# Optimization experiments

Measured on AMD Instinct MI355X. Metric: run time of the kernel, lower is better.

The kernel has to match this reference:

```python
import math
import jax, jax.numpy as jnp
import numpy as np

N_WL = 262144
T_REF = 273.15          # CONSTANTS.STANDARD_TEMPERATURE [K]
P_REF = 101325.0        # CONSTANTS.STANDARD_PRESSURE [Pa]
C_LIGHT = 2.99792458e8  # CONSTANTS.SPEED_OF_LIGHT
K_B = 1.380649e-23      # CONSTANTS.BOLTZMANN
N_AVO = 6.02214076e23   # CONSTANTS.AVOGADRO

# hard-coded line database: [center_wl, strength, width, temp_exp]; rows 0-2 O3, 3-5 H2O, 6-9 CO2
LINES = np.array([
    [254.0, 1.15e-17, 2.0, 0.05], [280.0, 5e-18, 3.0, 0.04], [310.0, 1.9e-19, 2.5, 0.03],
    [940.0, 2.5e-23, 3.0, 0.4],  [1130.0, 8.2e-24, 2.5, 0.35], [1380.0, 1.8e-22, 4.0, 0.45],
    [1400.0, 3.5e-25, 3.0, 0.5], [1600.0, 7.8e-26, 2.5, 0.48], [2000.0, 4.2e-24, 4.0, 0.52],
    [2700.0, 1.2e-24, 3.5, 0.49]], dtype=np.float32)
MASS = np.array([48.0]*3 + [18.0]*3 + [44.0]*4, dtype=np.float32)


def setup_inputs() -> dict:
    key = jax.random.key(0)
    ks = jax.random.split(key, 8)
    inp = {
        'wavelengths': jnp.linspace(200.0, 3000.0, N_WL, dtype=jnp.float32),
        'temperature': jnp.float32(250.0),
        'pressure': jnp.float32(80000.0),
        'conc_o3': jnp.float32(1e-6),
        'conc_h2o': jnp.float32(1e-2),
        'conc_co2': jnp.float32(4e-4),
        'mix_w1': jax.random.normal(ks[0], (10, 64), jnp.float32) * 0.3,
        'mix_b1': jnp.zeros((64,), jnp.float32),
        'mix_w2': jax.random.normal(ks[1], (64, 64), jnp.float32) * 0.12,
        'mix_b2': jnp.zeros((64,), jnp.float32),
        'mix_w3': jax.random.normal(ks[2], (64, N_WL), jnp.float32) * 0.12,
        'mix_b3': jnp.zeros((N_WL,), jnp.float32),
        'cont_w1': jax.random.normal(ks[3], (5, 32), jnp.float32) * 0.4,
        'cont_b1': jnp.zeros((32,), jnp.float32),
        'cont_w2': jax.random.normal(ks[4], (32, N_WL), jnp.float32) * 0.17,
        'cont_b2': jnp.zeros((N_WL,), jnp.float32),
    }
    return inp


def _voigt(wl, nu0, gamma_L, gamma_D):
    # wl: [N]; nu0, gamma_L, gamma_D: [L] -> returns [L, N]
    sigma = gamma_D / (math.sqrt(2.0 * math.log(2.0)) + 1e-12)          # [L]
    x = (wl[None, :] - nu0[:, None]) / (sigma[:, None] + 1e-12)          # [L,N]
    y = (gamma_L / (sigma + 1e-12))[:, None]                             # [L,1]
    t = y - 1j * x
    s = jnp.abs(x) + y
    mask1 = s >= 15.0
    mask2 = (s < 15.0) & (jnp.abs(x) >= 5.5)
    w1 = (t * 0.5641896 / (0.5 + t ** 2)).real
    u = t ** 2
    w2 = (t * (1.410474 + u * 0.5641896) / (0.75 + u * (3.0 + u))).real
    w3 = (jnp.exp(-x ** 2) * jnp.cos(2.0 * x * y) / math.sqrt(math.pi)
          + 2.0 * y / math.pi * jnp.sin(x ** 2) / (x ** 2 + y ** 2 + 1e-10))
    result = jnp.where(mask1, w1, jnp.where(mask2, w2, w3))
    return result / (sigma[:, None] * math.sqrt(math.pi) + 1e-12)


def reference(wavelengths, temperature, pressure, conc_o3, conc_h2o, conc_co2,
              mix_w1, mix_b1, mix_w2, mix_b2, mix_w3, mix_b3,
              cont_w1, cont_b1, cont_w2, cont_b2):
    lines = jnp.asarray(LINES)
    mass = jnp.asarray(MASS)
    conc = jnp.stack([conc_o3, conc_o3, conc_o3,
                      conc_h2o, conc_h2o, conc_h2o,
                      conc_co2, conc_co2, conc_co2, conc_co2])          # [10]
    nu0, strength, width, temp_exp = lines[:, 0], lines[:, 1], lines[:, 2], lines[:, 3]
    strength_T = strength * (T_REF / (temperature + 1e-12)) ** temp_exp  # [10]
    gamma_L = width * (pressure / (P_REF + 1e-12)) * jnp.sqrt(T_REF / (temperature + 1e-12))
    gamma_D = nu0 / C_LIGHT * jnp.sqrt(2.0 * K_B * temperature * N_AVO / (mass + 1e-12))

    profiles = _voigt(wavelengths, nu0, gamma_L, gamma_D)                # [10,N]
    cross = jnp.sum((conc * strength_T)[:, None] * profiles, axis=0)     # [N]

    # continuum net: 5 -> 32 (SiLU) -> N (softplus)
    cont_feat = jnp.stack([temperature / (T_REF + 1e-12),
                           pressure / (P_REF + 1e-12),
                           conc_h2o,
                           jnp.float32(1.0), jnp.float32(0.0)])
    h = jax.nn.silu(cont_feat @ cont_w1 + cont_b1)
    continuum = jax.nn.softplus(h @ cont_w2 + cont_b2)
    cross = cross + continuum

    # line-mixing net: 10 -> 64 (SiLU) -> 64 (SiLU) -> N (sigmoid); dropout is eval-mode identity
    mix_feat = jnp.concatenate([jnp.stack([temperature / (T_REF + 1e-12),
                                           pressure / (P_REF + 1e-12)]),
                                cross[:8]])
    m = jax.nn.silu(mix_feat @ mix_w1 + mix_b1)
    m = jax.nn.silu(m @ mix_w2 + mix_b2)
    mixing = jax.nn.sigmoid(m @ mix_w3 + mix_b3)
    return cross * (1.0 + 0.1 * (mixing - 0.5))
```

## Files before the change

### kernel.cpp

```cpp
#include <hip/hip_runtime.h>
#include <math.h>

#define N_WL 262144

#define T_REF 273.15
#define P_REF 101325.0
#define C_LIGHT 299792458.0
#define K_B 1.380649e-23
#define N_AVO 6.02214076e+23

__constant__ float c_nu0[10]  = {254.0f, 280.0f, 310.0f, 940.0f, 1130.0f, 1380.0f, 1400.0f, 1600.0f, 2000.0f, 2700.0f};
__constant__ float c_str[10]  = {1.15e-17f, 5e-18f, 1.9e-19f, 2.5e-23f, 8.2e-24f, 1.8e-22f, 3.5e-25f, 7.8e-26f, 4.2e-24f, 1.2e-24f};
__constant__ float c_wid[10]  = {2.0f, 3.0f, 2.5f, 3.0f, 2.5f, 4.0f, 3.0f, 2.5f, 4.0f, 3.5f};
__constant__ float c_texp[10] = {0.05f, 0.04f, 0.03f, 0.4f, 0.35f, 0.45f, 0.5f, 0.48f, 0.52f, 0.49f};
__constant__ float c_mass[10] = {48.f, 48.f, 48.f, 18.f, 18.f, 18.f, 44.f, 44.f, 44.f, 44.f};
__constant__ int   c_cidx[10] = {0, 0, 0, 1, 1, 1, 2, 2, 2, 2};

__device__ __forceinline__ float siluf(float x)     { return x / (1.0f + __expf(-x)); }
__device__ __forceinline__ float sigmoidf(float x)  { return 1.0f / (1.0f + __expf(-x)); }
__device__ __forceinline__ float softplusf(float x) { return fmaxf(x, 0.0f) + log1pf(expf(-fabsf(x))); }

__device__ __forceinline__ float voigt_w(float x, float y) {
    float ax = fabsf(x);
    float s  = ax + y;
    if (s >= 15.0f) {
        float ur = y * y - x * x;
        float ui = -2.0f * x * y;
        float dr = 0.5f + ur, di = ui;
        float nr = 0.5641896f * y, ni = 0.5641896f * (-x);
        float den = dr * dr + di * di;
        return (nr * dr + ni * di) / den;
    } else if (ax >= 5.5f) {
        float ur = y * y - x * x;
        float ui = -2.0f * x * y;
        float pr = 1.410474f + 0.5641896f * ur;
        float pi_ = 0.5641896f * ui;
        float tr = y, ti = -x;
        float nr = tr * pr - ti * pi_;
        float ni = tr * pi_ + ti * pr;
        float u2r = ur * ur - ui * ui;
        float u2i = 2.0f * ur * ui;
        float dr = 0.75f + 3.0f * ur + u2r;
        float di = 3.0f * ui + u2i;
        float den = dr * dr + di * di;
        return (nr * dr + ni * di) / den;
    } else {
        float x2 = x * x;
        return expf(-x2) * cosf(2.0f * x * y) * 0.5641895835477563f
             + (2.0f * y / 3.14159265358979f) * sinf(x2) / (x2 + y * y + 1e-10f);
    }
}

__global__ __launch_bounds__(256) void GasAbs_fused_kernel(
    const float* __restrict__ wl,
    const float* __restrict__ Tp, const float* __restrict__ Pp,
    const float* __restrict__ o3, const float* __restrict__ h2o, const float* __restrict__ co2,
    const float* __restrict__ mix_w1, const float* __restrict__ mix_b1,
    const float* __restrict__ mix_w2, const float* __restrict__ mix_b2,
    const float* __restrict__ mix_w3, const float* __restrict__ mix_b3,
    const float* __restrict__ cont_w1, const float* __restrict__ cont_b1,
    const float* __restrict__ cont_w2, const float* __restrict__ cont_b2,
    float* __restrict__ out)
{
    __shared__ float s_nu0[10], s_isig[10], s_y[10], s_scale[10];
    __shared__ float s_h[32];
    __shared__ float s_feat[10];
    __shared__ float s_m1[64];
    __shared__ float s_m2[64];

    const int t = threadIdx.x;

    if (t < 10) {
        const double T = (double)Tp[0];
        const double P = (double)Pp[0];
        const float cc3[3] = {o3[0], h2o[0], co2[0]};
        double nu0 = (double)c_nu0[t];
        double sT  = (double)c_str[t] * pow(T_REF / (T + 1e-12), (double)c_texp[t]);
        double gL  = (double)c_wid[t] * (P / (P_REF + 1e-12)) * sqrt(T_REF / (T + 1e-12));
        double gD  = nu0 / C_LIGHT * sqrt(2.0 * K_B * T * N_AVO / ((double)c_mass[t] + 1e-12));
        double sig = gD / (sqrt(2.0 * log(2.0)) + 1e-12);
        s_nu0[t]   = (float)nu0;
        s_isig[t]  = (float)(1.0 / (sig + 1e-12));
        s_y[t]     = (float)(gL / (sig + 1e-12));
        s_scale[t] = (float)((double)cc3[c_cidx[t]] * sT / (sig * sqrt(M_PI) + 1e-12));
    }
    if (t < 32) {
        const double T = (double)Tp[0];
        const double P = (double)Pp[0];
        float cf[5];
        cf[0] = (float)(T / (T_REF + 1e-12));
        cf[1] = (float)(P / (P_REF + 1e-12));
        cf[2] = h2o[0];
        cf[3] = 1.0f;
        cf[4] = 0.0f;
        float a = cont_b1[t];
        #pragma unroll
        for (int k = 0; k < 5; k++) a = fmaf(cf[k], cont_w1[k * 32 + t], a);
        s_h[t] = siluf(a);
    }
    __syncthreads();

    if (t < 8) {
        float w = wl[t];
        float c = cont_b2[t];
        #pragma unroll
        for (int j = 0; j < 32; j++) c = fmaf(s_h[j], cont_w2[(size_t)j * N_WL + t], c);
        float cross = softplusf(c);
        #pragma unroll
        for (int l = 0; l < 10; l++) {
            float x = (w - s_nu0[l]) * s_isig[l];
            cross = fmaf(s_scale[l], voigt_w(x, s_y[l]), cross);
        }
        s_feat[2 + t] = cross;
    }
    if (t == 0) {
        const double T = (double)Tp[0];
        const double P = (double)Pp[0];
        s_feat[0] = (float)(T / (T_REF + 1e-12));
        s_feat[1] = (float)(P / (P_REF + 1e-12));
    }
    __syncthreads();

    if (t < 64) {
        float a = mix_b1[t];
        #pragma unroll
        for (int k = 0; k < 10; k++) a = fmaf(s_feat[k], mix_w1[k * 64 + t], a);
        s_m1[t] = siluf(a);
    }
    __syncthreads();

    if (t < 64) {
        float a = mix_b2[t];
        #pragma unroll
        for (int k = 0; k < 64; k++) a = fmaf(s_m1[k], mix_w2[k * 64 + t], a);
        s_m2[t] = siluf(a);
    }
    __syncthreads();

    const int i0 = (blockIdx.x * 256 + t) * 4;

    const float4 w4 = *reinterpret_cast<const float4*>(wl + i0);

    float4 ac = *reinterpret_cast<const float4*>(cont_b2 + i0);
    #pragma unroll 16
    for (int j = 0; j < 32; j++) {
        const float hj = s_h[j];
        const float4 v = *reinterpret_cast<const float4*>(cont_w2 + (size_t)j * N_WL + i0);
        ac.x = fmaf(hj, v.x, ac.x);
        ac.y = fmaf(hj, v.y, ac.y);
        ac.z = fmaf(hj, v.z, ac.z);
        ac.w = fmaf(hj, v.w, ac.w);
    }

    float cr0 = softplusf(ac.x);
    float cr1 = softplusf(ac.y);
    float cr2 = softplusf(ac.z);
    float cr3 = softplusf(ac.w);

    #pragma unroll
    for (int l = 0; l < 10; l++) {
        const float nu0 = s_nu0[l], isig = s_isig[l], yy = s_y[l], sc = s_scale[l];
        cr0 = fmaf(sc, voigt_w((w4.x - nu0) * isig, yy), cr0);
        cr1 = fmaf(sc, voigt_w((w4.y - nu0) * isig, yy), cr1);
        cr2 = fmaf(sc, voigt_w((w4.z - nu0) * isig, yy), cr2);
        cr3 = fmaf(sc, voigt_w((w4.w - nu0) * isig, yy), cr3);
    }

    float4 am = *reinterpret_cast<const float4*>(mix_b3 + i0);
    #pragma unroll 16
    for (int j = 0; j < 64; j++) {
        const float mj = s_m2[j];
        const float4 v = *reinterpret_cast<const float4*>(mix_w3 + (size_t)j * N_WL + i0);
        am.x = fmaf(mj, v.x, am.x);
        am.y = fmaf(mj, v.y, am.y);
        am.z = fmaf(mj, v.z, am.z);
        am.w = fmaf(mj, v.w, am.w);
    }

    float4 o;
    o.x = cr0 * (0.95f + 0.1f * sigmoidf(am.x));
    o.y = cr1 * (0.95f + 0.1f * sigmoidf(am.y));
    o.z = cr2 * (0.95f + 0.1f * sigmoidf(am.z));
    o.w = cr3 * (0.95f + 0.1f * sigmoidf(am.w));
    *reinterpret_cast<float4*>(out + i0) = o;
}

extern "C" void kernel_launch(void* const* d_in, const int* in_sizes, int n_in,
                              void* d_out, int out_size, void* d_ws, size_t ws_size,
                              hipStream_t stream) {
    const float* wl      = (const float*)d_in[0];
    const float* Tp      = (const float*)d_in[1];
    const float* Pp      = (const float*)d_in[2];
    const float* o3      = (const float*)d_in[3];
    const float* h2o     = (const float*)d_in[4];
    const float* co2     = (const float*)d_in[5];
    const float* mix_w1  = (const float*)d_in[6];
    const float* mix_b1  = (const float*)d_in[7];
    const float* mix_w2  = (const float*)d_in[8];
    const float* mix_b2  = (const float*)d_in[9];
    const float* mix_w3  = (const float*)d_in[10];
    const float* mix_b3  = (const float*)d_in[11];
    const float* cont_w1 = (const float*)d_in[12];
    const float* cont_b1 = (const float*)d_in[13];
    const float* cont_w2 = (const float*)d_in[14];
    const float* cont_b2 = (const float*)d_in[15];
    float* out = (float*)d_out;

    const int threads = 256;
    const int blocks  = N_WL / (threads * 4);
    GasAbs_fused_kernel<<<blocks, threads, 0, stream>>>(
        wl, Tp, Pp, o3, h2o, co2,
        mix_w1, mix_b1, mix_w2, mix_b2, mix_w3, mix_b3,
        cont_w1, cont_b1, cont_w2, cont_b2, out);
}
```

Measured before the change: 153.8 us.

## Halve per-thread width and software-pipeline weight loads across Voigt compute

Each thread now handles 2 wavelengths instead of 4, doubling the block count from 256 to 512 so more of the GPU's compute units have work. Weight rows are loaded in batches of 8 float2s. The first batch of mix_w3 loads is issued before the Voigt computation so its memory latency overlaps that math, and each later batch is prefetched while the previous one is consumed. In exchange, every block repeats the small MLP prologue, which costs more in total, and the prefetch buffers raise register pressure.

```diff
diff --git a/kernel.cpp b/kernel.cpp
--- a/kernel.cpp
+++ b/kernel.cpp
@@ -137,52 +137,63 @@
     }
     __syncthreads();
 
-    const int i0 = (blockIdx.x * 256 + t) * 4;
-
-    const float4 w4 = *reinterpret_cast<const float4*>(wl + i0);
-
-    float4 ac = *reinterpret_cast<const float4*>(cont_b2 + i0);
-    #pragma unroll 16
-    for (int j = 0; j < 32; j++) {
-        const float hj = s_h[j];
-        const float4 v = *reinterpret_cast<const float4*>(cont_w2 + (size_t)j * N_WL + i0);
-        ac.x = fmaf(hj, v.x, ac.x);
-        ac.y = fmaf(hj, v.y, ac.y);
-        ac.z = fmaf(hj, v.z, ac.z);
-        ac.w = fmaf(hj, v.w, ac.w);
-    }
+    const int i0 = (blockIdx.x * 256 + t) * 2;
+
+    const float2 w2 = *reinterpret_cast<const float2*>(wl + i0);
+    float2 ac = *reinterpret_cast<const float2*>(cont_b2 + i0);
+    float2 am = *reinterpret_cast<const float2*>(mix_b3 + i0);
+
+    #pragma unroll
+    for (int jb = 0; jb < 32; jb += 8) {
+        float2 v[8];
+        #pragma unroll
+        for (int u = 0; u < 8; u++)
+            v[u] = *reinterpret_cast<const float2*>(cont_w2 + (size_t)(jb + u) * N_WL + i0);
+        #pragma unroll
+        for (int u = 0; u < 8; u++) {
+            const float hj = s_h[jb + u];
+            ac.x = fmaf(hj, v[u].x, ac.x);
+            ac.y = fmaf(hj, v[u].y, ac.y);
+        }
+    }
+
+    float2 vb[8];
+    #pragma unroll
+    for (int u = 0; u < 8; u++)
+        vb[u] = *reinterpret_cast<const float2*>(mix_w3 + (size_t)u * N_WL + i0);
 
     float cr0 = softplusf(ac.x);
     float cr1 = softplusf(ac.y);
-    float cr2 = softplusf(ac.z);
-    float cr3 = softplusf(ac.w);
 
     #pragma unroll
     for (int l = 0; l < 10; l++) {
         const float nu0 = s_nu0[l], isig = s_isig[l], yy = s_y[l], sc = s_scale[l];
-        cr0 = fmaf(sc, voigt_w((w4.x - nu0) * isig, yy), cr0);
-        cr1 = fmaf(sc, voigt_w((w4.y - nu0) * isig, yy), cr1);
-        cr2 = fmaf(sc, voigt_w((w4.z - nu0) * isig, yy), cr2);
-        cr3 = fmaf(sc, voigt_w((w4.w - nu0) * isig, yy), cr3);
-    }
-
-    float4 am = *reinterpret_cast<const float4*>(mix_b3 + i0);
-    #pragma unroll 16
-    for (int j = 0; j < 64; j++) {
-        const float mj = s_m2[j];
-        const float4 v = *reinterpret_cast<const float4*>(mix_w3 + (size_t)j * N_WL + i0);
-        am.x = fmaf(mj, v.x, am.x);
-        am.y = fmaf(mj, v.y, am.y);
-        am.z = fmaf(mj, v.z, am.z);
-        am.w = fmaf(mj, v.w, am.w);
-    }
-
-    float4 o;
+        cr0 = fmaf(sc, voigt_w((w2.x - nu0) * isig, yy), cr0);
+        cr1 = fmaf(sc, voigt_w((w2.y - nu0) * isig, yy), cr1);
+    }
+
+    #pragma unroll
+    for (int jb = 0; jb < 64; jb += 8) {
+        float2 vn[8];
+        if (jb + 8 < 64) {
+            #pragma unroll
+            for (int u = 0; u < 8; u++)
+                vn[u] = *reinterpret_cast<const float2*>(mix_w3 + (size_t)(jb + 8 + u) * N_WL + i0);
+        }
+        #pragma unroll
+        for (int u = 0; u < 8; u++) {
+            const float mj = s_m2[jb + u];
+            am.x = fmaf(mj, vb[u].x, am.x);
+            am.y = fmaf(mj, vb[u].y, am.y);
+        }
+        #pragma unroll
+        for (int u = 0; u < 8; u++) vb[u] = vn[u];
+    }
+
+    float2 o;
     o.x = cr0 * (0.95f + 0.1f * sigmoidf(am.x));
     o.y = cr1 * (0.95f + 0.1f * sigmoidf(am.y));
-    o.z = cr2 * (0.95f + 0.1f * sigmoidf(am.z));
-    o.w = cr3 * (0.95f + 0.1f * sigmoidf(am.w));
-    *reinterpret_cast<float4*>(out + i0) = o;
+    *reinterpret_cast<float2*>(out + i0) = o;
 }
 
 extern "C" void kernel_launch(void* const* d_in, const int* in_sizes, int n_in,
@@ -207,7 +218,7 @@
     float* out = (float*)d_out;
 
     const int threads = 256;
-    const int blocks  = N_WL / (threads * 4);
+    const int blocks  = N_WL / (threads * 2);
     GasAbs_fused_kernel<<<blocks, threads, 0, stream>>>(
         wl, Tp, Pp, o3, h2o, co2,
         mix_w1, mix_b1, mix_w2, mix_b2, mix_w3, mix_b3,
```

After: 163.2 us. 1.06x slower.

## Use one element per thread with a 16-deep register prefetch ring for weight streams

Applied to the files above, without the earlier changes.

Switches from four elements per thread via float4 loads to one element per thread, launching four times as many blocks. Weight rows from cont_w2 and mix_w3 are streamed through a 16-entry register ring that keeps loads in flight, and the Voigt evaluation is placed between the initial prefetch and the consumption loop to hide latency. Compiler barriers hold the load ordering. The aim is more memory-level parallelism and occupancy on this bandwidth-bound stream, at the cost of scalar loads and four times as many redundant per-block prologue MLP computations.

```diff
diff --git a/kernel.cpp b/kernel.cpp
--- a/kernel.cpp
+++ b/kernel.cpp
@@ -137,52 +137,48 @@
     }
     __syncthreads();
 
-    const int i0 = (blockIdx.x * 256 + t) * 4;
-
-    const float4 w4 = *reinterpret_cast<const float4*>(wl + i0);
-
-    float4 ac = *reinterpret_cast<const float4*>(cont_b2 + i0);
-    #pragma unroll 16
-    for (int j = 0; j < 32; j++) {
-        const float hj = s_h[j];
-        const float4 v = *reinterpret_cast<const float4*>(cont_w2 + (size_t)j * N_WL + i0);
-        ac.x = fmaf(hj, v.x, ac.x);
-        ac.y = fmaf(hj, v.y, ac.y);
-        ac.z = fmaf(hj, v.z, ac.z);
-        ac.w = fmaf(hj, v.w, ac.w);
-    }
-
-    float cr0 = softplusf(ac.x);
-    float cr1 = softplusf(ac.y);
-    float cr2 = softplusf(ac.z);
-    float cr3 = softplusf(ac.w);
-
+    const int i = blockIdx.x * 256 + t;
+    const float* __restrict__ wp = cont_w2 + i;
+    const float* __restrict__ mp = mix_w3  + i;
+
+    const float wv = wl[i];
+    const float bc = cont_b2[i];
+    const float bm = mix_b3[i];
+
+    float buf[16];
+    #pragma unroll
+    for (int k = 0; k < 16; k++)
+        buf[k] = wp[(size_t)k * N_WL];
+    asm volatile("" ::: "memory");
+
+    float vsum = 0.0f;
     #pragma unroll
     for (int l = 0; l < 10; l++) {
-        const float nu0 = s_nu0[l], isig = s_isig[l], yy = s_y[l], sc = s_scale[l];
-        cr0 = fmaf(sc, voigt_w((w4.x - nu0) * isig, yy), cr0);
-        cr1 = fmaf(sc, voigt_w((w4.y - nu0) * isig, yy), cr1);
-        cr2 = fmaf(sc, voigt_w((w4.z - nu0) * isig, yy), cr2);
-        cr3 = fmaf(sc, voigt_w((w4.w - nu0) * isig, yy), cr3);
-    }
-
-    float4 am = *reinterpret_cast<const float4*>(mix_b3 + i0);
-    #pragma unroll 16
-    for (int j = 0; j < 64; j++) {
-        const float mj = s_m2[j];
-        const float4 v = *reinterpret_cast<const float4*>(mix_w3 + (size_t)j * N_WL + i0);
-        am.x = fmaf(mj, v.x, am.x);
-        am.y = fmaf(mj, v.y, am.y);
-        am.z = fmaf(mj, v.z, am.z);
-        am.w = fmaf(mj, v.w, am.w);
-    }
-
-    float4 o;
-    o.x = cr0 * (0.95f + 0.1f * sigmoidf(am.x));
-    o.y = cr1 * (0.95f + 0.1f * sigmoidf(am.y));
-    o.z = cr2 * (0.95f + 0.1f * sigmoidf(am.z));
-    o.w = cr3 * (0.95f + 0.1f * sigmoidf(am.w));
-    *reinterpret_cast<float4*>(out + i0) = o;
+        const float x = (wv - s_nu0[l]) * s_isig[l];
+        vsum = fmaf(s_scale[l], voigt_w(x, s_y[l]), vsum);
+    }
+
+    float acc_c = bc;
+    float acc_m = bm;
+
+    #pragma unroll
+    for (int g = 0; g < 12; g++) {
+        #pragma unroll
+        for (int u = 0; u < 8; u++) {
+            const int k = g * 8 + u;
+            const float v = buf[k & 15];
+            if (k < 32) acc_c = fmaf(s_h[k],      v, acc_c);
+            else        acc_m = fmaf(s_m2[k - 32], v, acc_m);
+            const int kn = k + 16;
+            if (kn < 96)
+                buf[k & 15] = (kn < 32) ? wp[(size_t)kn * N_WL]
+                                        : mp[(size_t)(kn - 32) * N_WL];
+        }
+        asm volatile("" ::: "memory");
+    }
+
+    const float cross = softplusf(acc_c) + vsum;
+    out[i] = cross * (0.95f + 0.1f * sigmoidf(acc_m));
 }
 
 extern "C" void kernel_launch(void* const* d_in, const int* in_sizes, int n_in,
@@ -207,7 +203,7 @@
     float* out = (float*)d_out;
 
     const int threads = 256;
-    const int blocks  = N_WL / (threads * 4);
+    const int blocks  = N_WL / threads;
     GasAbs_fused_kernel<<<blocks, threads, 0, stream>>>(
         wl, Tp, Pp, o3, h2o, co2,
         mix_w1, mix_b1, mix_w2, mix_b2, mix_w3, mix_b3,
```

Result: no change. 150.8 us (median of 2 runs) (-1.9%).

## Split fused kernel into prep, split-K atomic accumulation, and finish kernels

Applied to the files above, without the earlier changes.

The single fused kernel is split into three launches. A prep kernel computes the small MLP hidden states and line parameters into a workspace and zeroes the accumulators. A split-K accumulation kernel spreads the 96-row weight GEMV over 3072 blocks, each handling 4 rows, and combines partial sums with float atomics. A finish kernel applies the Voigt profiles and activations. The goal is to raise parallelism over the original 256 blocks, each of which streamed all 96 weight rows. In exchange it adds two extra launches, roughly 16 MB of atomic read-modify-write traffic, and a run-to-run nondeterministic summation order.

```diff
diff --git a/kernel.cpp b/kernel.cpp
--- a/kernel.cpp
+++ b/kernel.cpp
@@ -8,6 +8,14 @@
 #define C_LIGHT 299792458.0
 #define K_B 1.380649e-23
 #define N_AVO 6.02214076e+23
+
+#define WS_H     0
+#define WS_M2    32
+#define WS_NU0   96
+#define WS_ISIG  106
+#define WS_Y     116
+#define WS_SCALE 126
+#define WS_ACC   256
 
 __constant__ float c_nu0[10]  = {254.0f, 280.0f, 310.0f, 940.0f, 1130.0f, 1380.0f, 1400.0f, 1600.0f, 2000.0f, 2700.0f};
 __constant__ float c_str[10]  = {1.15e-17f, 5e-18f, 1.9e-19f, 2.5e-23f, 8.2e-24f, 1.8e-22f, 3.5e-25f, 7.8e-26f, 4.2e-24f, 1.2e-24f};
@@ -51,24 +59,29 @@
     }
 }
 
-__global__ __launch_bounds__(256) void GasAbs_fused_kernel(
+__global__ __launch_bounds__(256) void GasAbs_prep_kernel(
     const float* __restrict__ wl,
     const float* __restrict__ Tp, const float* __restrict__ Pp,
     const float* __restrict__ o3, const float* __restrict__ h2o, const float* __restrict__ co2,
     const float* __restrict__ mix_w1, const float* __restrict__ mix_b1,
     const float* __restrict__ mix_w2, const float* __restrict__ mix_b2,
-    const float* __restrict__ mix_w3, const float* __restrict__ mix_b3,
     const float* __restrict__ cont_w1, const float* __restrict__ cont_b1,
     const float* __restrict__ cont_w2, const float* __restrict__ cont_b2,
-    float* __restrict__ out)
+    float* __restrict__ ws)
 {
+    const int t = threadIdx.x;
+
+    if (blockIdx.x != 0) {
+        const int idx = (blockIdx.x - 1) * 256 + t;
+        float4 z = {0.f, 0.f, 0.f, 0.f};
+        reinterpret_cast<float4*>(ws + WS_ACC)[idx] = z;
+        return;
+    }
+
     __shared__ float s_nu0[10], s_isig[10], s_y[10], s_scale[10];
     __shared__ float s_h[32];
     __shared__ float s_feat[10];
     __shared__ float s_m1[64];
-    __shared__ float s_m2[64];
-
-    const int t = threadIdx.x;
 
     if (t < 10) {
         const double T = (double)Tp[0];
@@ -83,6 +96,10 @@
         s_isig[t]  = (float)(1.0 / (sig + 1e-12));
         s_y[t]     = (float)(gL / (sig + 1e-12));
         s_scale[t] = (float)((double)cc3[c_cidx[t]] * sT / (sig * sqrt(M_PI) + 1e-12));
+        ws[WS_NU0  + t] = s_nu0[t];
+        ws[WS_ISIG + t] = s_isig[t];
+        ws[WS_Y    + t] = s_y[t];
+        ws[WS_SCALE+ t] = s_scale[t];
     }
     if (t < 32) {
         const double T = (double)Tp[0];
@@ -97,6 +114,7 @@
         #pragma unroll
         for (int k = 0; k < 5; k++) a = fmaf(cf[k], cont_w1[k * 32 + t], a);
         s_h[t] = siluf(a);
+        ws[WS_H + t] = s_h[t];
     }
     __syncthreads();
 
@@ -133,55 +151,111 @@
         float a = mix_b2[t];
         #pragma unroll
         for (int k = 0; k < 64; k++) a = fmaf(s_m1[k], mix_w2[k * 64 + t], a);
-        s_m2[t] = siluf(a);
-    }
+        ws[WS_M2 + t] = siluf(a);
+    }
+}
+
+#define RPB   4
+#define CHUNK 2048
+__global__ __launch_bounds__(256) void GasAbs_acc_kernel(
+    const float* __restrict__ cont_w2,
+    const float* __restrict__ mix_w3,
+    float* __restrict__ ws)
+{
+    const int g = blockIdx.x >> 7;
+    const int c = blockIdx.x & 127;
+    const int base = c * CHUNK + threadIdx.x * 8;
+
+    const float* W;
+    const float* coef;
+    float* plane;
+    int row0;
+    if (g < 8) {
+        row0  = g * RPB;
+        W     = cont_w2;
+        coef  = ws + WS_H + row0;
+        plane = ws + WS_ACC;
+    } else {
+        row0  = (g - 8) * RPB;
+        W     = mix_w3;
+        coef  = ws + WS_M2 + row0;
+        plane = ws + WS_ACC + N_WL;
+    }
+
+    const float k0 = coef[0], k1 = coef[1], k2 = coef[2], k3 = coef[3];
+
+    float4 v0[RPB], v1[RPB];
+    #pragma unroll
+    for (int r = 0; r < RPB; ++r) {
+        const float* p = W + (size_t)(row0 + r) * N_WL + base;
+        v0[r] = *reinterpret_cast<const float4*>(p);
+        v1[r] = *reinterpret_cast<const float4*>(p + 4);
+    }
+
+    float4 a0 = {0.f,0.f,0.f,0.f}, a1 = {0.f,0.f,0.f,0.f};
+    const float kk[RPB] = {k0, k1, k2, k3};
+    #pragma unroll
+    for (int r = 0; r < RPB; ++r) {
+        a0.x = fmaf(kk[r], v0[r].x, a0.x);
+        a0.y = fmaf(kk[r], v0[r].y, a0.y);
+        a0.z = fmaf(kk[r], v0[r].z, a0.z);
+        a0.w = fmaf(kk[r], v0[r].w, a0.w);
+        a1.x = fmaf(kk[r], v1[r].x, a1.x);
+        a1.y = fmaf(kk[r], v1[r].y, a1.y);
+        a1.z = fmaf(kk[r], v1[r].z, a1.z);
+        a1.w = fmaf(kk[r], v1[r].w, a1.w);
+    }
+
+    float* d = plane + base;
+    atomicAdd(d + 0, a0.x);
+    atomicAdd(d + 1, a0.y);
+    atomicAdd(d + 2, a0.z);
+    atomicAdd(d + 3, a0.w);
+    atomicAdd(d + 4, a1.x);
+    atomicAdd(d + 5, a1.y);
+    atomicAdd(d + 6, a1.z);
+    atomicAdd(d + 7, a1.w);
+}
+
+__global__ __launch_bounds__(256) void GasAbs_finish_kernel(
+    const float* __restrict__ wl,
+    const float* __restrict__ mix_b3,
+    const float* __restrict__ cont_b2,
+    const float* __restrict__ ws,
+    float* __restrict__ out)
+{
+    __shared__ float sp[40];
+    const int t = threadIdx.x;
+    if (t < 40) sp[t] = ws[WS_NU0 + t];
     __syncthreads();
 
     const int i0 = (blockIdx.x * 256 + t) * 4;
 
-    const float4 w4 = *reinterpret_cast<const float4*>(wl + i0);
-
-    float4 ac = *reinterpret_cast<const float4*>(cont_b2 + i0);
-    #pragma unroll 16
-    for (int j = 0; j < 32; j++) {
-        const float hj = s_h[j];
-        const float4 v = *reinterpret_cast<const float4*>(cont_w2 + (size_t)j * N_WL + i0);
-        ac.x = fmaf(hj, v.x, ac.x);
-        ac.y = fmaf(hj, v.y, ac.y);
-        ac.z = fmaf(hj, v.z, ac.z);
-        ac.w = fmaf(hj, v.w, ac.w);
-    }
-
-    float cr0 = softplusf(ac.x);
-    float cr1 = softplusf(ac.y);
-    float cr2 = softplusf(ac.z);
-    float cr3 = softplusf(ac.w);
+    const float4 w4  = *reinterpret_cast<const float4*>(wl + i0);
+    const float4 bc4 = *reinterpret_cast<const float4*>(cont_b2 + i0);
+    const float4 bm4 = *reinterpret_cast<const float4*>(mix_b3 + i0);
+    const float4 aC  = *reinterpret_cast<const float4*>(ws + WS_ACC + i0);
+    const float4 aM  = *reinterpret_cast<const float4*>(ws + WS_ACC + N_WL + i0);
+
+    float cr0 = softplusf(bc4.x + aC.x);
+    float cr1 = softplusf(bc4.y + aC.y);
+    float cr2 = softplusf(bc4.z + aC.z);
+    float cr3 = softplusf(bc4.w + aC.w);
 
     #pragma unroll
     for (int l = 0; l < 10; l++) {
-        const float nu0 = s_nu0[l], isig = s_isig[l], yy = s_y[l], sc = s_scale[l];
+        const float nu0 = sp[l], isig = sp[10 + l], yy = sp[20 + l], sc = sp[30 + l];
         cr0 = fmaf(sc, voigt_w((w4.x - nu0) * isig, yy), cr0);
         cr1 = fmaf(sc, voigt_w((w4.y - nu0) * isig, yy), cr1);
         cr2 = fmaf(sc, voigt_w((w4.z - nu0) * isig, yy), cr2);
         cr3 = fmaf(sc, voigt_w((w4.w - nu0) * isig, yy), cr3);
     }
 
-    float4 am = *reinterpret_cast<const float4*>(mix_b3 + i0);
-    #pragma unroll 16
-    for (int j = 0; j < 64; j++) {
-        const float mj = s_m2[j];
-        const float4 v = *reinterpret_cast<const float4*>(mix_w3 + (size_t)j * N_WL + i0);
-        am.x = fmaf(mj, v.x, am.x);
-        am.y = fmaf(mj, v.y, am.y);
-        am.z = fmaf(mj, v.z, am.z);
-        am.w = fmaf(mj, v.w, am.w);
-    }
-
     float4 o;
-    o.x = cr0 * (0.95f + 0.1f * sigmoidf(am.x));
-    o.y = cr1 * (0.95f + 0.1f * sigmoidf(am.y));
-    o.z = cr2 * (0.95f + 0.1f * sigmoidf(am.z));
-    o.w = cr3 * (0.95f + 0.1f * sigmoidf(am.w));
+    o.x = cr0 * (0.95f + 0.1f * sigmoidf(bm4.x + aM.x));
+    o.y = cr1 * (0.95f + 0.1f * sigmoidf(bm4.y + aM.y));
+    o.z = cr2 * (0.95f + 0.1f * sigmoidf(bm4.z + aM.z));
+    o.w = cr3 * (0.95f + 0.1f * sigmoidf(bm4.w + aM.w));
     *reinterpret_cast<float4*>(out + i0) = o;
 }
 
@@ -204,12 +278,16 @@
     const float* cont_b1 = (const float*)d_in[13];
     const float* cont_w2 = (const float*)d_in[14];
     const float* cont_b2 = (const float*)d_in[15];
+    float* ws  = (float*)d_ws;
     float* out = (float*)d_out;
 
-    const int threads = 256;
-    const int blocks  = N_WL / (threads * 4);
-    GasAbs_fused_kernel<<<blocks, threads, 0, stream>>>(
+    GasAbs_prep_kernel<<<513, 256, 0, stream>>>(
         wl, Tp, Pp, o3, h2o, co2,
-        mix_w1, mix_b1, mix_w2, mix_b2, mix_w3, mix_b3,
-        cont_w1, cont_b1, cont_w2, cont_b2, out);
-}
+        mix_w1, mix_b1, mix_w2, mix_b2,
+        cont_w1, cont_b1, cont_w2, cont_b2, ws);
+
+    GasAbs_acc_kernel<<<24 * 128, 256, 0, stream>>>(cont_w2, mix_w3, ws);
+
+    GasAbs_finish_kernel<<<N_WL / (256 * 4), 256, 0, stream>>>(
+        wl, mix_b3, cont_b2, ws, out);
+}
```

Result: slower. 306.4 us (+99.2%).
